# Kernel optimization log

Measured on AMD Instinct MI355X. Metric: run time of the kernel, lower is better.

## Reference

```python
import jax, jax.numpy as jnp
import numpy as np
from jax import lax


def setup_inputs() -> dict:
    key = jax.random.key(0)
    k1, k2 = jax.random.split(key)
    B, C, H, W = 4, 64, 64, 64
    foreground = jax.random.normal(k1, (B, C, H, W), dtype=jnp.float32)
    masks = jax.random.uniform(k2, (B, 1, H, W), dtype=jnp.float32)
    return {"foreground": foreground, "masks": masks}


def reference(foreground, masks):
    # First-call path of KnowledgeConsistentAttention (att_scores_prev is None).
    # patch_size=3 -> padding=1 around 1x1 dynamic kernels; propagate_size=3 -> 3x3 sum pool.
    B, C, H, W = foreground.shape
    P = H * W
    # Dynamic 1x1 kernels: one per spatial location, L2-normalized over channels.
    K = foreground.reshape(B, C, P).transpose(0, 2, 1)            # [B, P, C]
    norm = jnp.sqrt(jnp.sum(K * K, axis=2, keepdims=True))        # flatten(1).norm per kernel
    K = K / (norm + 1e-8)
    # conv2d with 1x1 kernels and padding=1 == GEMM over zero-padded input.
    Xpad = jnp.pad(foreground, ((0, 0), (0, 0), (1, 1), (1, 1)))  # [B, C, H+2, W+2]
    scores = jnp.einsum('bpc,bchw->bphw', K, Xpad)                # [B, P, H+2, W+2]
    # avg_pool2d(k=3, stride=1, pad=1) * 9 == zero-padded 3x3 sum pool.
    scores = lax.reduce_window(scores, jnp.float32(0.0), lax.add,
                               (1, 1, 3, 3), (1, 1, 1, 1), 'SAME')
    attn = jax.nn.softmax(scores, axis=1)                          # softmax over P kernels
    # conv_transpose2d with 1x1 kernels, padding=1 crops the border back to HxW.
    out = jnp.einsum('bphw,bpc->bchw', attn[:, :, 1:-1, 1:-1], K)  # [B, C, H, W]
    return out
```

## Files before the change

kernel.cpp:

```cpp
#include <hip/hip_runtime.h>
#include <hip/hip_bf16.h>
#include <math.h>

#define Bn 4
#define Cn 64
#define Pn 4096
#define QT 64
#define PBK 128
#define NITER (Pn / PBK)
#define LOG2E 1.4426950408889634f

typedef __attribute__((ext_vector_type(8))) short short8;
typedef __attribute__((ext_vector_type(4))) short short4v;
typedef __attribute__((ext_vector_type(4))) float float4v;
typedef unsigned short bfu;

__device__ __forceinline__ bfu f2bf(float x) {
    unsigned u = __float_as_uint(x);
    u = (u + 0x7fffu + ((u >> 16) & 1u)) >> 16;
    return (bfu)u;
}

__global__ __launch_bounds__(256) void prep_kernel(const float* __restrict__ fg,
                                                   bfu* __restrict__ Kpc,
                                                   bfu* __restrict__ Kcp2,
                                                   float* __restrict__ S) {
    __shared__ float shbuf[64 * 64];
    int t = threadIdx.x;
    if (blockIdx.x < 512) {
        float* tile  = shbuf;
        float* rnorm = shbuf + 64 * 33;
        int b  = blockIdx.x >> 7;
        int p0 = (blockIdx.x & 127) << 5;
        const float* src = fg + (size_t)b * Cn * Pn + p0;
        #pragma unroll
        for (int i = 0; i < 8; ++i) {
            int idx = i * 256 + t;
            int c = idx >> 5, p = idx & 31;
            tile[c * 33 + p] = src[(size_t)c * Pn + p];
        }
        __syncthreads();
        if (t < 32) {
            float ss = 0.f;
            #pragma unroll
            for (int c = 0; c < 64; ++c) { float v = tile[c * 33 + t]; ss += v * v; }
            rnorm[t] = 1.0f / (sqrtf(ss) + 1e-8f);
        }
        __syncthreads();
        bfu* dpc = Kpc + ((size_t)b * Pn + p0) * Cn;
        #pragma unroll
        for (int i = 0; i < 8; ++i) {
            int idx = i * 256 + t;
            int p = idx >> 6, c = idx & 63;
            dpc[(size_t)p * Cn + c] = f2bf(tile[c * 33 + p] * rnorm[p]);
        }
        bfu* d2 = Kcp2 + ((size_t)b * 256 + (p0 >> 4)) * 1024;
        #pragma unroll
        for (int i = 0; i < 8; ++i) {
            int idx = i * 256 + t;
            int c = idx >> 5, p = idx & 31;
            d2[(size_t)(p >> 4) * 1024 + c * 16 + (p & 15)] =
                f2bf(tile[c * 33 + p] * rnorm[p]);
        }
    } else {
        float (*pl)[64] = (float(*)[64])shbuf;
        int bc = blockIdx.x - 512;
        const float* src = fg + (size_t)bc * Pn;
        float*       dst = S  + (size_t)bc * Pn;
        #pragma unroll
        for (int i = 0; i < 16; ++i) {
            int idx = i * 256 + t;
            pl[idx >> 6][idx & 63] = src[idx];
        }
        __syncthreads();
        #pragma unroll
        for (int i = 0; i < 16; ++i) {
            int idx = i * 256 + t;
            int h = idx >> 6, w = idx & 63;
            float s = 0.f;
            #pragma unroll
            for (int dh = -1; dh <= 1; ++dh) {
                int hh = h + dh;
                if (hh < 0 || hh >= 64) continue;
                #pragma unroll
                for (int dw = -1; dw <= 1; ++dw) {
                    int ww = w + dw;
                    if (ww < 0 || ww >= 64) continue;
                    s += pl[hh][ww];
                }
            }
            dst[idx] = s * LOG2E;
        }
    }
}

__global__ __launch_bounds__(512, 1) void flash_kernel(const bfu* __restrict__ Kpc,
                                                       const bfu* __restrict__ Kcp2,
                                                       const float* __restrict__ S,
                                                       float* __restrict__ out) {
    __shared__ __align__(16) bfu smem[33792];
    __shared__ float wredl[8][QT];
    bfu* Sl = smem;

    int i  = blockIdx.x;
    int b  = (i & 7) >> 1;
    int qt = ((i >> 3) << 1) | (i & 1);
    int q0 = qt * QT;
    int t  = threadIdx.x;
    int w = t >> 6, l = t & 63, lq = l & 15, quad = l >> 4;

    const float* Sg  = S    + (size_t)b * Cn * Pn;
    const bfu*   gpc = Kpc  + (size_t)b * Pn * Cn;
    const bfu*   gt  = Kcp2 + (size_t)b * 256 * 1024;

    {
        int c = t >> 3, qq = (t & 7) * 8;
        const float* sp = &Sg[(size_t)c * Pn + q0 + qq];
        float4 v0 = *(const float4*)sp;
        float4 v1 = *(const float4*)(sp + 4);
        float vv[8] = {v0.x, v0.y, v0.z, v0.w, v1.x, v1.y, v1.z, v1.w};
        int ch = c >> 3, cl = c & 7;
        #pragma unroll
        for (int k = 0; k < 8; ++k) {
            int row = qq + k;
            Sl[row * 64 + ((ch ^ (row & 7)) << 3) + cl] = f2bf(vv[k]);
        }
    }
    __syncthreads();

    short8 bs[4][2];
    #pragma unroll
    for (int nt = 0; nt < 4; ++nt)
        #pragma unroll
        for (int ks = 0; ks < 2; ++ks) {
            int row = nt * 16 + lq;
            bs[nt][ks] = *(const short8*)&Sl[row * 64 + (((ks * 4 + quad) ^ (lq & 7)) << 3)];
        }

    float4v o[4][4];
    #pragma unroll
    for (int nt = 0; nt < 4; ++nt)
        #pragma unroll
        for (int cb = 0; cb < 4; ++cb) o[nt][cb] = (float4v){0.f, 0.f, 0.f, 0.f};
    float lacc[4] = {0.f, 0.f, 0.f, 0.f};

    const bfu* ap = gpc + ((size_t)16 * w + lq) * Cn + quad * 8;
    const bfu* tp = gt + (size_t)w * 1024 + lq * 16 + quad * 4;

    float4 a0 = *(const float4*)ap;
    float4 a1 = *(const float4*)(ap + 32);
    short4v kb[4];
    #pragma unroll
    for (int cb = 0; cb < 4; ++cb) kb[cb] = *(const short4v*)(tp + cb * 256);

    for (int pb = 0; pb < NITER; ++pb) {
        float4 na0, na1;
        short4v nkb[4];
        if (pb + 1 < NITER) {
            const bfu* apn = ap + (size_t)(pb + 1) * PBK * Cn;
            na0 = *(const float4*)apn;
            na1 = *(const float4*)(apn + 32);
            const bfu* tpn = tp + (size_t)(pb + 1) * 8 * 1024;
            #pragma unroll
            for (int cb = 0; cb < 4; ++cb) nkb[cb] = *(const short4v*)(tpn + cb * 256);
        }

        short8 af0 = *(short8*)&a0, af1 = *(short8*)&a1;
        float4v sc[4];
        #pragma unroll
        for (int nt = 0; nt < 4; ++nt) {
            float4v acc = (float4v){0.f, 0.f, 0.f, 0.f};
            acc = __builtin_amdgcn_mfma_f32_16x16x32_bf16(af0, bs[nt][0], acc, 0, 0, 0);
            acc = __builtin_amdgcn_mfma_f32_16x16x32_bf16(af1, bs[nt][1], acc, 0, 0, 0);
            sc[nt] = acc;
        }

        short4v epk[4];
        #pragma unroll
        for (int nt = 0; nt < 4; ++nt) {
            float e0 = __builtin_amdgcn_exp2f(sc[nt][0]);
            float e1 = __builtin_amdgcn_exp2f(sc[nt][1]);
            float e2 = __builtin_amdgcn_exp2f(sc[nt][2]);
            float e3 = __builtin_amdgcn_exp2f(sc[nt][3]);
            lacc[nt] += (e0 + e1) + (e2 + e3);
            short4v ep = {(short)f2bf(e0), (short)f2bf(e1), (short)f2bf(e2), (short)f2bf(e3)};
            epk[nt] = ep;
        }

        #pragma unroll
        for (int cb = 0; cb < 4; ++cb) {
            #pragma unroll
            for (int nt = 0; nt < 4; ++nt)
                o[nt][cb] = __builtin_amdgcn_mfma_f32_16x16x16bf16_1k(epk[nt], kb[cb], o[nt][cb], 0, 0, 0);
        }

        a0 = na0; a1 = na1;
        #pragma unroll
        for (int cb = 0; cb < 4; ++cb) kb[cb] = nkb[cb];
    }

    #pragma unroll
    for (int nt = 0; nt < 4; ++nt) {
        lacc[nt] += __shfl_xor(lacc[nt], 16);
        lacc[nt] += __shfl_xor(lacc[nt], 32);
    }
    if (quad == 0)
        #pragma unroll
        for (int nt = 0; nt < 4; ++nt) wredl[w][nt * 16 + lq] = lacc[nt];

    float* Ol = (float*)smem;
    __syncthreads();
    if (w < 4) {
        #pragma unroll
        for (int nt = 0; nt < 4; ++nt)
            #pragma unroll
            for (int cb = 0; cb < 4; ++cb)
                #pragma unroll
                for (int r = 0; r < 4; ++r)
                    Ol[(w * 64 + 16 * cb + lq) * 66 + nt * 16 + quad * 4 + r] = o[nt][cb][r];
    }
    __syncthreads();
    if (w >= 4) {
        #pragma unroll
        for (int nt = 0; nt < 4; ++nt)
            #pragma unroll
            for (int cb = 0; cb < 4; ++cb)
                #pragma unroll
                for (int r = 0; r < 4; ++r)
                    Ol[((w - 4) * 64 + 16 * cb + lq) * 66 + nt * 16 + quad * 4 + r] += o[nt][cb][r];
    }
    __syncthreads();

    float* og = out + (size_t)b * Cn * Pn;
    #pragma unroll
    for (int k = 0; k < 8; ++k) {
        int idx = k * 512 + t;
        int c = idx >> 6, q = idx & 63;
        float lsum = ((wredl[0][q] + wredl[1][q]) + (wredl[2][q] + wredl[3][q])) +
                     ((wredl[4][q] + wredl[5][q]) + (wredl[6][q] + wredl[7][q]));
        float v = ((Ol[c * 66 + q] + Ol[(64 + c) * 66 + q]) +
                   (Ol[(128 + c) * 66 + q] + Ol[(192 + c) * 66 + q])) / lsum;
        og[(size_t)c * Pn + q0 + q] = v;
    }
}

extern "C" void kernel_launch(void* const* d_in, const int* in_sizes, int n_in,
                              void* d_out, int out_size, void* d_ws, size_t ws_size,
                              hipStream_t stream) {
    const float* fg = (const float*)d_in[0];
    float* out = (float*)d_out;
    bfu*   Kpc  = (bfu*)d_ws;
    bfu*   Kcp2 = Kpc + (size_t)Bn * Pn * Cn;
    float* S    = (float*)(Kcp2 + (size_t)Bn * Pn * Cn);

    prep_kernel <<<768, 256, 0, stream>>>(fg, Kpc, Kcp2, S);
    flash_kernel<<<Bn * 64, 512, 0, stream>>>(Kpc, Kcp2, S, out);
}
```

Measured before the change: 92.44 us.

## Stream K tiles through triple-buffered LDS with async global-to-LDS loads

```diff
diff --git a/kernel.cpp b/kernel.cpp
--- a/kernel.cpp
+++ b/kernel.cpp
@@ -10,6 +10,10 @@
 #define NITER (Pn / PBK)
 #define LOG2E 1.4426950408889634f
 
+#define STG_BUF 32768
+#define SL_OFF  98304
+#define SMEM_BYTES 106496
+
 typedef __attribute__((ext_vector_type(8))) short short8;
 typedef __attribute__((ext_vector_type(4))) short short4v;
 typedef __attribute__((ext_vector_type(4))) float float4v;
@@ -19,6 +23,12 @@
     unsigned u = __float_as_uint(x);
     u = (u + 0x7fffu + ((u >> 16) & 1u)) >> 16;
     return (bfu)u;
+}
+
+__device__ __forceinline__ void gl16(const bfu* g, void* l) {
+    __builtin_amdgcn_global_load_lds(
+        (const __attribute__((address_space(1))) void*)g,
+        (__attribute__((address_space(3))) void*)l, 16, 0, 0);
 }
 
 __global__ __launch_bounds__(256) void prep_kernel(const float* __restrict__ fg,
@@ -98,9 +108,9 @@
                                                        const bfu* __restrict__ Kcp2,
                                                        const float* __restrict__ S,
                                                        float* __restrict__ out) {
-    __shared__ __align__(16) bfu smem[33792];
+    __shared__ __align__(16) unsigned char smem[SMEM_BYTES];
     __shared__ float wredl[8][QT];
-    bfu* Sl = smem;
+    bfu* Sl = (bfu*)(smem + SL_OFF);
 
     int i  = blockIdx.x;
     int b  = (i & 7) >> 1;
@@ -144,28 +154,46 @@
         for (int cb = 0; cb < 4; ++cb) o[nt][cb] = (float4v){0.f, 0.f, 0.f, 0.f};
     float lacc[4] = {0.f, 0.f, 0.f, 0.f};
 
-    const bfu* ap = gpc + ((size_t)16 * w + lq) * Cn + quad * 8;
-    const bfu* tp = gt + (size_t)w * 1024 + lq * 16 + quad * 4;
-
-    float4 a0 = *(const float4*)ap;
-    float4 a1 = *(const float4*)(ap + 32);
-    short4v kb[4];
-    #pragma unroll
-    for (int cb = 0; cb < 4; ++cb) kb[cb] = *(const short4v*)(tp + cb * 256);
+    int l8 = l >> 3, l7 = l & 7;
+    int aoff = l8 * 64 + (((l7 ^ l8)) << 3);
+    int toff = l * 8;
+    int abyte0 = lq * 128 + (((quad)     ^ (lq & 7)) << 4);
+    int abyte1 = lq * 128 + (((4 + quad) ^ (lq & 7)) << 4);
+    int tbyte  = 16384 + lq * 32 + quad * 8;
+
+    unsigned wb = (unsigned)w * 2048;
+    unsigned ro = 0 * STG_BUF, mo = 1 * STG_BUF, io = 2 * STG_BUF;
+
+    #define ISSUE(tile, boff)                                                      \
+    {                                                                              \
+        const bfu* gA = gpc + ((size_t)(tile) * PBK + (size_t)w * 16) * 64;        \
+        const bfu* gT = gt + ((size_t)(tile) * 8 + w) * 1024;                      \
+        gl16(gA + aoff,       smem + (boff) + wb);                                 \
+        gl16(gA + 512 + aoff, smem + (boff) + wb + 1024);                          \
+        gl16(gT + toff,       smem + (boff) + 16384 + wb);                         \
+        gl16(gT + 512 + toff, smem + (boff) + 16384 + wb + 1024);                  \
+    }
+
+    ISSUE(0, ro);
+    ISSUE(1, mo);
 
     for (int pb = 0; pb < NITER; ++pb) {
-        float4 na0, na1;
-        short4v nkb[4];
-        if (pb + 1 < NITER) {
-            const bfu* apn = ap + (size_t)(pb + 1) * PBK * Cn;
-            na0 = *(const float4*)apn;
-            na1 = *(const float4*)(apn + 32);
-            const bfu* tpn = tp + (size_t)(pb + 1) * 8 * 1024;
-            #pragma unroll
-            for (int cb = 0; cb < 4; ++cb) nkb[cb] = *(const short4v*)(tpn + cb * 256);
-        }
-
-        short8 af0 = *(short8*)&a0, af1 = *(short8*)&a1;
+        if (pb < NITER - 2) {
+            ISSUE(pb + 2, io);
+            asm volatile("s_waitcnt vmcnt(8)" ::: "memory");
+        } else if (pb == NITER - 2) {
+            asm volatile("s_waitcnt vmcnt(4)" ::: "memory");
+        } else {
+            asm volatile("s_waitcnt vmcnt(0)" ::: "memory");
+        }
+
+        short8 af0 = *(const short8*)(smem + ro + wb + abyte0);
+        short8 af1 = *(const short8*)(smem + ro + wb + abyte1);
+        short4v kb[4];
+        #pragma unroll
+        for (int cb = 0; cb < 4; ++cb)
+            kb[cb] = *(const short4v*)(smem + ro + wb * 0 + (unsigned)w * 2048 + tbyte + cb * 512);
+
         float4v sc[4];
         #pragma unroll
         for (int nt = 0; nt < 4; ++nt) {
@@ -194,10 +222,9 @@
                 o[nt][cb] = __builtin_amdgcn_mfma_f32_16x16x16bf16_1k(epk[nt], kb[cb], o[nt][cb], 0, 0, 0);
         }
 
-        a0 = na0; a1 = na1;
-        #pragma unroll
-        for (int cb = 0; cb < 4; ++cb) kb[cb] = nkb[cb];
-    }
+        unsigned tmp = ro; ro = mo; mo = io; io = tmp;
+    }
+    #undef ISSUE
 
     #pragma unroll
     for (int nt = 0; nt < 4; ++nt) {
```

Result: slower. 94.90 us (+2.7%).

## Split attention key range in two halves and combine partial results

Applied to the files above, without the earlier changes.

```diff
diff --git a/kernel.cpp b/kernel.cpp
--- a/kernel.cpp
+++ b/kernel.cpp
@@ -7,7 +7,8 @@
 #define Pn 4096
 #define QT 64
 #define PBK 128
-#define NITER (Pn / PBK)
+#define PHALF 2048
+#define NITER (PHALF / PBK)
 #define LOG2E 1.4426950408889634f
 
 typedef __attribute__((ext_vector_type(8))) short short8;
@@ -94,24 +95,27 @@
     }
 }
 
-__global__ __launch_bounds__(512, 1) void flash_kernel(const bfu* __restrict__ Kpc,
+__global__ __launch_bounds__(512, 4) void flash_kernel(const bfu* __restrict__ Kpc,
                                                        const bfu* __restrict__ Kcp2,
                                                        const float* __restrict__ S,
-                                                       float* __restrict__ out) {
+                                                       float* __restrict__ Opart,
+                                                       float* __restrict__ lpart) {
     __shared__ __align__(16) bfu smem[33792];
     __shared__ float wredl[8][QT];
     bfu* Sl = smem;
 
-    int i  = blockIdx.x;
-    int b  = (i & 7) >> 1;
-    int qt = ((i >> 3) << 1) | (i & 1);
+    int i    = blockIdx.x;
+    int half = i >> 8;
+    int j    = i & 255;
+    int b  = (j & 7) >> 1;
+    int qt = ((j >> 3) << 1) | (j & 1);
     int q0 = qt * QT;
     int t  = threadIdx.x;
     int w = t >> 6, l = t & 63, lq = l & 15, quad = l >> 4;
 
     const float* Sg  = S    + (size_t)b * Cn * Pn;
-    const bfu*   gpc = Kpc  + (size_t)b * Pn * Cn;
-    const bfu*   gt  = Kcp2 + (size_t)b * 256 * 1024;
+    const bfu*   gpc = Kpc  + (size_t)b * Pn * Cn + (size_t)half * PHALF * Cn;
+    const bfu*   gt  = Kcp2 + (size_t)b * 256 * 1024 + (size_t)half * 128 * 1024;
 
     {
         int c = t >> 3, qq = (t & 7) * 8;
@@ -231,17 +235,39 @@
     }
     __syncthreads();
 
-    float* og = out + (size_t)b * Cn * Pn;
+    float* Og = Opart + (size_t)(half * Bn + b) * Cn * Pn;
     #pragma unroll
     for (int k = 0; k < 8; ++k) {
         int idx = k * 512 + t;
         int c = idx >> 6, q = idx & 63;
-        float lsum = ((wredl[0][q] + wredl[1][q]) + (wredl[2][q] + wredl[3][q])) +
-                     ((wredl[4][q] + wredl[5][q]) + (wredl[6][q] + wredl[7][q]));
         float v = ((Ol[c * 66 + q] + Ol[(64 + c) * 66 + q]) +
-                   (Ol[(128 + c) * 66 + q] + Ol[(192 + c) * 66 + q])) / lsum;
-        og[(size_t)c * Pn + q0 + q] = v;
-    }
+                   (Ol[(128 + c) * 66 + q] + Ol[(192 + c) * 66 + q]));
+        Og[(size_t)c * Pn + q0 + q] = v;
+    }
+    if (t < QT) {
+        float ls = ((wredl[0][t] + wredl[1][t]) + (wredl[2][t] + wredl[3][t])) +
+                   ((wredl[4][t] + wredl[5][t]) + (wredl[6][t] + wredl[7][t]));
+        lpart[(size_t)(half * Bn + b) * Pn + q0 + t] = ls;
+    }
+}
+
+__global__ __launch_bounds__(256) void combine_kernel(const float* __restrict__ Opart,
+                                                      const float* __restrict__ lpart,
+                                                      float* __restrict__ out) {
+    const int BCP = Bn * Cn * Pn;
+    int idx = (blockIdx.x * 256 + threadIdx.x) * 4;
+    int b = idx >> 18;
+    int q = idx & (Pn - 1);
+    float4 o0 = *(const float4*)(Opart + idx);
+    float4 o1 = *(const float4*)(Opart + BCP + idx);
+    float4 l0 = *(const float4*)(lpart + (size_t)b * Pn + q);
+    float4 l1 = *(const float4*)(lpart + (size_t)(Bn + b) * Pn + q);
+    float4 r;
+    r.x = (o0.x + o1.x) / (l0.x + l1.x);
+    r.y = (o0.y + o1.y) / (l0.y + l1.y);
+    r.z = (o0.z + o1.z) / (l0.z + l1.z);
+    r.w = (o0.w + o1.w) / (l0.w + l1.w);
+    *(float4*)(out + idx) = r;
 }
 
 extern "C" void kernel_launch(void* const* d_in, const int* in_sizes, int n_in,
@@ -249,10 +275,13 @@
                               hipStream_t stream) {
     const float* fg = (const float*)d_in[0];
     float* out = (float*)d_out;
-    bfu*   Kpc  = (bfu*)d_ws;
-    bfu*   Kcp2 = Kpc + (size_t)Bn * Pn * Cn;
-    float* S    = (float*)(Kcp2 + (size_t)Bn * Pn * Cn);
-
-    prep_kernel <<<768, 256, 0, stream>>>(fg, Kpc, Kcp2, S);
-    flash_kernel<<<Bn * 64, 512, 0, stream>>>(Kpc, Kcp2, S, out);
-}
+    bfu*   Kpc   = (bfu*)d_ws;
+    bfu*   Kcp2  = Kpc + (size_t)Bn * Pn * Cn;
+    float* S     = (float*)(Kcp2 + (size_t)Bn * Pn * Cn);
+    float* Opart = S + (size_t)Bn * Cn * Pn;
+    float* lpart = Opart + 2 * (size_t)Bn * Cn * Pn;
+
+    prep_kernel   <<<768, 256, 0, stream>>>(fg, Kpc, Kcp2, S);
+    flash_kernel  <<<512, 512, 0, stream>>>(Kpc, Kcp2, S, Opart, lpart);
+    combine_kernel<<<1024, 256, 0, stream>>>(Opart, lpart, out);
+}
```

New measurement: 124.8 us. 35.0% more time.

## Double query tile per block with two wave groups sharing K streams

Applied to the files above, without the earlier changes.

```diff
diff --git a/kernel.cpp b/kernel.cpp
--- a/kernel.cpp
+++ b/kernel.cpp
@@ -5,7 +5,7 @@
 #define Bn 4
 #define Cn 64
 #define Pn 4096
-#define QT 64
+#define QT 128
 #define PBK 128
 #define NITER (Pn / PBK)
 #define LOG2E 1.4426950408889634f
@@ -13,6 +13,7 @@
 typedef __attribute__((ext_vector_type(8))) short short8;
 typedef __attribute__((ext_vector_type(4))) short short4v;
 typedef __attribute__((ext_vector_type(4))) float float4v;
+typedef __attribute__((ext_vector_type(2))) unsigned uint2v;
 typedef unsigned short bfu;
 
 __device__ __forceinline__ bfu f2bf(float x) {
@@ -94,13 +95,13 @@
     }
 }
 
-__global__ __launch_bounds__(512, 1) void flash_kernel(const bfu* __restrict__ Kpc,
-                                                       const bfu* __restrict__ Kcp2,
-                                                       const float* __restrict__ S,
-                                                       float* __restrict__ out) {
-    __shared__ __align__(16) bfu smem[33792];
-    __shared__ float wredl[8][QT];
-    bfu* Sl = smem;
+__global__ __launch_bounds__(1024, 4) void flash_kernel(const bfu* __restrict__ Kpc,
+                                                        const bfu* __restrict__ Kcp2,
+                                                        const float* __restrict__ S,
+                                                        float* __restrict__ out) {
+    __shared__ __align__(16) unsigned char smem[135168];
+    __shared__ float wredl[16][64];
+    bfu* Sl = (bfu*)smem;
 
     int i  = blockIdx.x;
     int b  = (i & 7) >> 1;
@@ -108,13 +109,14 @@
     int q0 = qt * QT;
     int t  = threadIdx.x;
     int w = t >> 6, l = t & 63, lq = l & 15, quad = l >> 4;
+    int g = w >> 3, pw = w & 7;
 
     const float* Sg  = S    + (size_t)b * Cn * Pn;
     const bfu*   gpc = Kpc  + (size_t)b * Pn * Cn;
     const bfu*   gt  = Kcp2 + (size_t)b * 256 * 1024;
 
     {
-        int c = t >> 3, qq = (t & 7) * 8;
+        int c = t >> 4, qq = (t & 15) * 8;
         const float* sp = &Sg[(size_t)c * Pn + q0 + qq];
         float4 v0 = *(const float4*)sp;
         float4 v1 = *(const float4*)(sp + 4);
@@ -133,7 +135,7 @@
     for (int nt = 0; nt < 4; ++nt)
         #pragma unroll
         for (int ks = 0; ks < 2; ++ks) {
-            int row = nt * 16 + lq;
+            int row = g * 64 + nt * 16 + lq;
             bs[nt][ks] = *(const short8*)&Sl[row * 64 + (((ks * 4 + quad) ^ (lq & 7)) << 3)];
         }
 
@@ -144,8 +146,8 @@
         for (int cb = 0; cb < 4; ++cb) o[nt][cb] = (float4v){0.f, 0.f, 0.f, 0.f};
     float lacc[4] = {0.f, 0.f, 0.f, 0.f};
 
-    const bfu* ap = gpc + ((size_t)16 * w + lq) * Cn + quad * 8;
-    const bfu* tp = gt + (size_t)w * 1024 + lq * 16 + quad * 4;
+    const bfu* ap = gpc + ((size_t)16 * pw + lq) * Cn + quad * 8;
+    const bfu* tp = gt + (size_t)pw * 1024 + lq * 16 + quad * 4;
 
     float4 a0 = *(const float4*)ap;
     float4 a1 = *(const float4*)(ap + 32);
@@ -153,6 +155,7 @@
     #pragma unroll
     for (int cb = 0; cb < 4; ++cb) kb[cb] = *(const short4v*)(tp + cb * 256);
 
+    #pragma unroll 2
     for (int pb = 0; pb < NITER; ++pb) {
         float4 na0, na1;
         short4v nkb[4];
@@ -183,8 +186,11 @@
             float e2 = __builtin_amdgcn_exp2f(sc[nt][2]);
             float e3 = __builtin_amdgcn_exp2f(sc[nt][3]);
             lacc[nt] += (e0 + e1) + (e2 + e3);
-            short4v ep = {(short)f2bf(e0), (short)f2bf(e1), (short)f2bf(e2), (short)f2bf(e3)};
-            epk[nt] = ep;
+            unsigned plo, phi;
+            asm("v_cvt_pk_bf16_f32 %0, %1, %2" : "=v"(plo) : "v"(e0), "v"(e1));
+            asm("v_cvt_pk_bf16_f32 %0, %1, %2" : "=v"(phi) : "v"(e2), "v"(e3));
+            uint2v pk2 = {plo, phi};
+            epk[nt] = __builtin_bit_cast(short4v, pk2);
         }
 
         #pragma unroll
@@ -208,38 +214,44 @@
         #pragma unroll
         for (int nt = 0; nt < 4; ++nt) wredl[w][nt * 16 + lq] = lacc[nt];
 
-    float* Ol = (float*)smem;
-    __syncthreads();
-    if (w < 4) {
+    float* Ol  = (float*)smem;
+    float* Olg = Ol + g * 16896;
+    int lw = w & 7;
+    __syncthreads();
+    if (lw < 4) {
         #pragma unroll
         for (int nt = 0; nt < 4; ++nt)
             #pragma unroll
             for (int cb = 0; cb < 4; ++cb)
                 #pragma unroll
                 for (int r = 0; r < 4; ++r)
-                    Ol[(w * 64 + 16 * cb + lq) * 66 + nt * 16 + quad * 4 + r] = o[nt][cb][r];
-    }
-    __syncthreads();
-    if (w >= 4) {
+                    Olg[(lw * 64 + 16 * cb + lq) * 66 + nt * 16 + quad * 4 + r] = o[nt][cb][r];
+    }
+    __syncthreads();
+    if (lw >= 4) {
         #pragma unroll
         for (int nt = 0; nt < 4; ++nt)
             #pragma unroll
             for (int cb = 0; cb < 4; ++cb)
                 #pragma unroll
                 for (int r = 0; r < 4; ++r)
-                    Ol[((w - 4) * 64 + 16 * cb + lq) * 66 + nt * 16 + quad * 4 + r] += o[nt][cb][r];
+                    Olg[((lw - 4) * 64 + 16 * cb + lq) * 66 + nt * 16 + quad * 4 + r] += o[nt][cb][r];
     }
     __syncthreads();
 
     float* og = out + (size_t)b * Cn * Pn;
     #pragma unroll
     for (int k = 0; k < 8; ++k) {
-        int idx = k * 512 + t;
-        int c = idx >> 6, q = idx & 63;
-        float lsum = ((wredl[0][q] + wredl[1][q]) + (wredl[2][q] + wredl[3][q])) +
-                     ((wredl[4][q] + wredl[5][q]) + (wredl[6][q] + wredl[7][q]));
-        float v = ((Ol[c * 66 + q] + Ol[(64 + c) * 66 + q]) +
-                   (Ol[(128 + c) * 66 + q] + Ol[(192 + c) * 66 + q])) / lsum;
+        int idx = k * 1024 + t;
+        int c = idx >> 7, q = idx & 127;
+        int g2 = q >> 6, ql = q & 63;
+        const float* O2 = Ol + g2 * 16896;
+        float lsum = ((wredl[g2 * 8 + 0][ql] + wredl[g2 * 8 + 1][ql]) +
+                      (wredl[g2 * 8 + 2][ql] + wredl[g2 * 8 + 3][ql])) +
+                     ((wredl[g2 * 8 + 4][ql] + wredl[g2 * 8 + 5][ql]) +
+                      (wredl[g2 * 8 + 6][ql] + wredl[g2 * 8 + 7][ql]));
+        float v = ((O2[c * 66 + ql] + O2[(64 + c) * 66 + ql]) +
+                   (O2[(128 + c) * 66 + ql] + O2[(192 + c) * 66 + ql])) / lsum;
         og[(size_t)c * Pn + q0 + q] = v;
     }
 }
@@ -254,5 +266,5 @@
     float* S    = (float*)(Kcp2 + (size_t)Bn * Pn * Cn);
 
     prep_kernel <<<768, 256, 0, stream>>>(fg, Kpc, Kcp2, S);
-    flash_kernel<<<Bn * 64, 512, 0, stream>>>(Kpc, Kcp2, S, out);
-}
+    flash_kernel<<<128, 1024, 0, stream>>>(Kpc, Kcp2, S, out);
+}
```

Measured after the change: 325.0 us. 3.52x slower.
